# Performance work log

Measured on AMD Instinct MI355X. Metric: run time of the kernel, lower is better.

## Reference

```python
import jax, jax.numpy as jnp
import numpy as np
from functools import partial

B, A = 256, 32          # batch_size, num_atoms
N = B * A               # total nodes = 8192
E = 262144              # edges
H = 128                 # hidden_dim
LD, AF = 64, 16         # latent_dim, atom_feature_dim
L = 6                   # num_layers
LN_EPS = 1e-5

silu = jax.nn.silu


def setup_inputs() -> dict:
    key = jax.random.key(0)
    ks = jax.random.split(key, 32)
    s = 0.02
    inp = {
        "z": jax.random.normal(ks[0], (B, LD), jnp.float32),
        "atom_types": jax.random.uniform(ks[1], (N, AF), jnp.float32),
        "pos_init": jax.random.normal(ks[2], (N, 3), jnp.float32) * 0.1,
        "edge_index": jax.random.randint(ks[3], (2, E), 0, N, jnp.int64) if jax.config.jax_enable_x64 else jax.random.randint(ks[3], (2, E), 0, N, jnp.int32),
        "batch": jax.random.randint(ks[4], (N,), 0, B, jnp.int32),
        # latent injector: (LD+AF)->2H -> 2H->H -> H->H
        "inj_W1": jax.random.normal(ks[5], (LD + AF, 2 * H), jnp.float32) * s,
        "inj_b1": jnp.zeros((2 * H,), jnp.float32),
        "inj_W2": jax.random.normal(ks[6], (2 * H, H), jnp.float32) * s,
        "inj_b2": jnp.zeros((H,), jnp.float32),
        "inj_W3": jax.random.normal(ks[7], (H, H), jnp.float32) * s,
        "inj_b3": jnp.zeros((H,), jnp.float32),
        # stacked per-layer params [L, ...]
        "edge_W1": jax.random.normal(ks[8], (L, 2 * H + 1, H), jnp.float32) * s,
        "edge_b1": jnp.zeros((L, H), jnp.float32),
        "edge_W2": jax.random.normal(ks[9], (L, H, H), jnp.float32) * s,
        "edge_b2": jnp.zeros((L, H), jnp.float32),
        "node_W1": jax.random.normal(ks[10], (L, 2 * H, H), jnp.float32) * s,
        "node_b1": jnp.zeros((L, H), jnp.float32),
        "node_W2": jax.random.normal(ks[11], (L, H, H), jnp.float32) * s,
        "node_b2": jnp.zeros((L, H), jnp.float32),
        "coord_W1": jax.random.normal(ks[12], (L, H, H), jnp.float32) * s,
        "coord_b1": jnp.zeros((L, H), jnp.float32),
        "coord_W2": jax.random.normal(ks[13], (L, H, 1), jnp.float32) * s,  # no bias
        "ln_g": jnp.ones((L, H), jnp.float32),
        "ln_b": jnp.zeros((L, H), jnp.float32),
    }
    return inp


def _layer_norm(x, g, b):
    mu = jnp.mean(x, axis=-1, keepdims=True)
    var = jnp.mean(jnp.square(x - mu), axis=-1, keepdims=True)
    return (x - mu) * jax.lax.rsqrt(var + LN_EPS) * g + b


def _egnn_forward(z, atom_types, pos_init, row, col,
                  inj_W1, inj_b1, inj_W2, inj_b2, inj_W3, inj_b3,
                  edge_W1, edge_b1, edge_W2, edge_b2,
                  node_W1, node_b1, node_W2, node_b2,
                  coord_W1, coord_b1, coord_W2, ln_g, ln_b):
    # latent injection
    z_exp = jnp.repeat(z, A, axis=0)                      # [N, LD]
    h0 = jnp.concatenate([atom_types, z_exp], axis=1)     # [N, AF+LD]
    h = silu(h0 @ inj_W1 + inj_b1)
    h = silu(h @ inj_W2 + inj_b2)
    h = h @ inj_W3 + inj_b3                               # [N, H]

    deg = jax.ops.segment_sum(jnp.ones((E,), h.dtype), row, num_segments=N)[:, None]  # [N,1]

    def step(carry, p):
        h, pos = carry
        (eW1, eb1, eW2, eb2, nW1, nb1, nW2, nb2, cW1, cb1, cW2, g, b) = p
        dpos = pos[row] - pos[col]                                   # [E,3]
        dist_sq = jnp.sum(jnp.square(dpos), axis=1, keepdims=True)   # [E,1]
        ef = jnp.concatenate([h[row], h[col], dist_sq], axis=1)      # [E,2H+1]
        m = silu(silu(ef @ eW1 + eb1) @ eW2 + eb2)                   # [E,H]
        cw = silu(m @ cW1 + cb1) @ cW2                               # [E,1]
        coord_update = jax.ops.segment_sum(cw * dpos, row, num_segments=N)  # [N,3]
        pos_new = pos + coord_update / (deg + 1e-6)
        agg = jax.ops.segment_sum(m, row, num_segments=N)            # [N,H]
        nu = silu(jnp.concatenate([h, agg], axis=1) @ nW1 + nb1) @ nW2 + nb2
        h_new = _layer_norm(h + nu, g, b)
        return (h_new, pos_new), None

    params = (edge_W1, edge_b1, edge_W2, edge_b2, node_W1, node_b1,
              node_W2, node_b2, coord_W1, coord_b1, coord_W2, ln_g, ln_b)
    (h, pos), _ = jax.lax.scan(step, (h, pos_init), params)
    return pos


def reference(z, atom_types, pos_init, edge_index, batch,
              inj_W1, inj_b1, inj_W2, inj_b2, inj_W3, inj_b3,
              edge_W1, edge_b1, edge_W2, edge_b2,
              node_W1, node_b1, node_W2, node_b2,
              coord_W1, coord_b1, coord_W2, ln_g, ln_b):
    row, col = edge_index[0], edge_index[1]
    return _egnn_forward(z, atom_types, pos_init, row, col,
                         inj_W1, inj_b1, inj_W2, inj_b2, inj_W3, inj_b3,
                         edge_W1, edge_b1, edge_W2, edge_b2,
                         node_W1, node_b1, node_W2, node_b2,
                         coord_W1, coord_b1, coord_W2, ln_g, ln_b)
```

## Files before the change

### kernel.cpp

```cpp
#include <hip/hip_runtime.h>
#include <hip/hip_bf16.h>

#define NNODES 8192
#define NEDGES 262144
#define HDIM 128
#define NLAYERS 6
#define NMASK (NNODES - 1)

typedef __attribute__((ext_vector_type(8))) short bf16x8;
typedef __attribute__((ext_vector_type(4))) float f32x4;

__device__ __forceinline__ float silu_f(float x) {
    return x * __builtin_amdgcn_rcpf(1.0f + __expf(-x));
}
__device__ __forceinline__ unsigned short f2bu(float x) {
    unsigned int u; __builtin_memcpy(&u, &x, 4);
    return (unsigned short)((u + 0x8000u) >> 16);
}
__device__ __forceinline__ float bu2f(unsigned short u) {
    unsigned int v = ((unsigned int)u) << 16;
    float f; __builtin_memcpy(&f, &v, 4);
    return f;
}

__global__ void detect_kernel(const int* __restrict__ ei32, int* __restrict__ flags) {
    if (blockIdx.x == 0 && threadIdx.x == 0) {
        flags[1] = (ei32[1] == 0 && ei32[3] == 0 && ei32[5] == 0 && ei32[7] == 0) ? 1 : 0;
    }
}
__device__ __forceinline__ int load_idx(const void* ei, int is64, int i) {
    int v = is64 ? (int)(((const long long*)ei)[i]) : ((const int*)ei)[i];
    return v & NMASK;
}

__global__ void pos_init_kernel(const float* __restrict__ pin, float* __restrict__ pos) {
    int i = blockIdx.x * blockDim.x + threadIdx.x;
    if (i < NNODES * 3) pos[i] = pin[i];
}

__global__ void cnt_kernel(const void* __restrict__ ei, const int* __restrict__ flags,
                           int* __restrict__ cnt) {
    int i = blockIdx.x * blockDim.x + threadIdx.x;
    if (i < NEDGES) atomicAdd(&cnt[load_idx(ei, flags[1], i)], 1);
}
__global__ void scan_kernel(const int* __restrict__ cnt, int* __restrict__ woff,
                            float* __restrict__ deg) {
    __shared__ int sums[256];
    const int t = threadIdx.x;
    const int base = t * 32;
    int s = 0;
#pragma unroll
    for (int i = 0; i < 32; ++i) s += cnt[base + i];
    sums[t] = s;
    __syncthreads();
    if (t == 0) {
        int run = 0;
        for (int k = 0; k < 256; ++k) { int v = sums[k]; sums[k] = run; run += v; }
    }
    __syncthreads();
    int run = sums[t];
#pragma unroll
    for (int i = 0; i < 32; ++i) {
        int c = cnt[base + i];
        woff[base + i] = run;
        deg[base + i] = (float)c;
        run += c;
    }
}
__global__ void scatter_kernel(const void* __restrict__ ei, const int* __restrict__ flags,
                               int* __restrict__ woff,
                               int* __restrict__ rowS, int* __restrict__ colS) {
    int i = blockIdx.x * blockDim.x + threadIdx.x;
    if (i < NEDGES) {
        const int is64 = flags[1];
        int r = load_idx(ei, is64, i);
        int c = load_idx(ei, is64, NEDGES + i);
        int p = atomicAdd(&woff[r], 1);
        rowS[p] = r;
        colS[p] = c;
    }
}

__global__ void prep_weights_kernel(const float* __restrict__ eW1,
                                    const float* __restrict__ eW2,
                                    const float* __restrict__ cW1,
                                    const float* __restrict__ nW1,
                                    const float* __restrict__ nW2,
                                    unsigned short* __restrict__ ewt,
                                    unsigned short* __restrict__ n1tb,
                                    unsigned short* __restrict__ n2tb,
                                    float* __restrict__ w1d) {
    const int TB = NLAYERS * 8 * 4 * 128 * 8;
    const int TS = NLAYERS * 4 * 4 * 128 * 8;
    const int TD = NLAYERS * 128;
    const int TOT = 2 * TB + 3 * TS + TD;
    for (int i = blockIdx.x * blockDim.x + threadIdx.x; i < TOT;
         i += gridDim.x * blockDim.x) {
        if (i < TB) {
            int j = i & 7, r = i >> 3;
            int n = r & 127; r >>= 7;
            int ch = r & 3; r >>= 2;
            int sl = r & 7; int l = r >> 3;
            int k = sl * 32 + ch * 8 + j;
            ewt[(size_t)(l * 16 + sl) * 4096 + ch * 1024 + n * 8 + j] =
                f2bu(eW1[((size_t)l * 257 + k) * 128 + n]);
        } else if (i < TB + TS) {
            int q = i - TB;
            int j = q & 7, r = q >> 3;
            int n = r & 127; r >>= 7;
            int ch = r & 3; r >>= 2;
            int sl = r & 3; int l = r >> 2;
            int k = sl * 32 + ch * 8 + j;
            ewt[(size_t)(l * 16 + 8 + sl) * 4096 + ch * 1024 + n * 8 + j] =
                f2bu(eW2[((size_t)l * 128 + k) * 128 + n]);
        } else if (i < TB + 2 * TS) {
            int q = i - TB - TS;
            int j = q & 7, r = q >> 3;
            int n = r & 127; r >>= 7;
            int ch = r & 3; r >>= 2;
            int sl = r & 3; int l = r >> 2;
            int k = sl * 32 + ch * 8 + j;
            ewt[(size_t)(l * 16 + 12 + sl) * 4096 + ch * 1024 + n * 8 + j] =
                f2bu(cW1[((size_t)l * 128 + k) * 128 + n]);
        } else if (i < 2 * TB + 2 * TS) {
            int q = i - TB - 2 * TS;
            int j = q & 7, r = q >> 3;
            int n = r & 127; r >>= 7;
            int ch = r & 3; r >>= 2;
            int sl = r & 7; int l = r >> 3;
            int k = sl * 32 + ch * 8 + j;
            n1tb[q] = f2bu(nW1[((size_t)l * 256 + k) * 128 + n]);
        } else if (i < 2 * TB + 3 * TS) {
            int q = i - 2 * TB - 2 * TS;
            int j = q & 7, r = q >> 3;
            int n = r & 127; r >>= 7;
            int ch = r & 3; r >>= 2;
            int sl = r & 3; int l = r >> 2;
            int k = sl * 32 + ch * 8 + j;
            n2tb[q] = f2bu(nW2[((size_t)l * 128 + k) * 128 + n]);
        } else {
            int r = i - 2 * TB - 3 * TS, l = r / 128, n = r % 128;
            w1d[r] = eW1[((size_t)l * 257 + 256) * 128 + n];
        }
    }
}

__global__ __launch_bounds__(256) void inj_kernel(
    const float* __restrict__ atom, const float* __restrict__ z,
    const float* __restrict__ W1, const float* __restrict__ b1,
    const float* __restrict__ W2, const float* __restrict__ b2,
    const float* __restrict__ W3, const float* __restrict__ b3,
    unsigned short* __restrict__ hb)
{
    __shared__ __align__(16) float in_s[16][84];
    __shared__ __align__(16) float s1[16][260];
    __shared__ __align__(16) float s2[16][132];
    const int tid = threadIdx.x;
    const int n0 = blockIdx.x * 16;

    if (tid < 80) {
        for (int e = 0; e < 16; ++e) {
            int n = n0 + e;
            in_s[e][tid] = (tid < 16) ? atom[n * 16 + tid] : z[(n >> 5) * 64 + (tid - 16)];
        }
    }
    __syncthreads();
    {
        float acc[16];
        float bias = b1[tid];
#pragma unroll
        for (int e = 0; e < 16; ++e) acc[e] = bias;
        for (int k4 = 0; k4 < 20; ++k4) {
            float w0 = W1[(k4 * 4 + 0) * 256 + tid];
            float w1 = W1[(k4 * 4 + 1) * 256 + tid];
            float w2 = W1[(k4 * 4 + 2) * 256 + tid];
            float w3 = W1[(k4 * 4 + 3) * 256 + tid];
#pragma unroll
            for (int e = 0; e < 16; ++e) {
                const float4 v = *(const float4*)&in_s[e][k4 * 4];
                acc[e] += v.x * w0 + v.y * w1 + v.z * w2 + v.w * w3;
            }
        }
#pragma unroll
        for (int e = 0; e < 16; ++e) s1[e][tid] = silu_f(acc[e]);
    }
    __syncthreads();
    const int j = tid & 127, hv = tid >> 7;
    {
        float acc[8];
        float bias = b2[j];
#pragma unroll
        for (int e = 0; e < 8; ++e) acc[e] = bias;
        for (int k4 = 0; k4 < 64; ++k4) {
            float w0 = W2[(k4 * 4 + 0) * 128 + j];
            float w1 = W2[(k4 * 4 + 1) * 128 + j];
            float w2 = W2[(k4 * 4 + 2) * 128 + j];
            float w3 = W2[(k4 * 4 + 3) * 128 + j];
#pragma unroll
            for (int e = 0; e < 8; ++e) {
                const float4 v = *(const float4*)&s1[hv * 8 + e][k4 * 4];
                acc[e] += v.x * w0 + v.y * w1 + v.z * w2 + v.w * w3;
            }
        }
#pragma unroll
        for (int e = 0; e < 8; ++e) s2[hv * 8 + e][j] = silu_f(acc[e]);
    }
    __syncthreads();
    {
        float acc[8];
        float bias = b3[j];
#pragma unroll
        for (int e = 0; e < 8; ++e) acc[e] = bias;
        for (int k4 = 0; k4 < 32; ++k4) {
            float w0 = W3[(k4 * 4 + 0) * 128 + j];
            float w1 = W3[(k4 * 4 + 1) * 128 + j];
            float w2 = W3[(k4 * 4 + 2) * 128 + j];
            float w3 = W3[(k4 * 4 + 3) * 128 + j];
#pragma unroll
            for (int e = 0; e < 8; ++e) {
                const float4 v = *(const float4*)&s2[hv * 8 + e][k4 * 4];
                acc[e] += v.x * w0 + v.y * w1 + v.z * w2 + v.w * w3;
            }
        }
#pragma unroll
        for (int e = 0; e < 8; ++e)
            hb[(size_t)(n0 + hv * 8 + e) * HDIM + j] = f2bu(acc[e]);
    }
}

__global__ __launch_bounds__(256, 3) void edge_mfma_kernel(
    const unsigned short* __restrict__ hb, const float* __restrict__ pos,
    const int* __restrict__ rowS, const int* __restrict__ colS,
    const unsigned short* __restrict__ wt,
    const float* __restrict__ w1d,
    const float* __restrict__ eb1, const float* __restrict__ eb2,
    const float* __restrict__ cb1, const float* __restrict__ cw2,
    float* __restrict__ agg, float* __restrict__ cu)
{
    __shared__ __align__(16) unsigned short Cbuf[128][136];

    const int tid = threadIdx.x;
    const int e0 = blockIdx.x * 128;
    const int L = tid & 63;
    const int w = tid >> 6;
    const int quad = L >> 4, l16 = L & 15;
    const int m0 = w * 32;

    const unsigned short* bbase = wt + quad * 1024 + l16 * 8;

    bf16x8 breg[2][8];
    bf16x8 areg[2][2];
#pragma unroll
    for (int nt = 0; nt < 8; ++nt)
        breg[0][nt] = *(const bf16x8*)(bbase + nt * 128);

    if (tid < 128) {
        int r = rowS[e0 + tid], c = colS[e0 + tid];
        float dx = pos[r * 3 + 0] - pos[c * 3 + 0];
        float dy = pos[r * 3 + 1] - pos[c * 3 + 1];
        float dz = pos[r * 3 + 2] - pos[c * 3 + 2];
        *(float*)&Cbuf[tid][128] = dx * dx + dy * dy + dz * dz;
        Cbuf[tid][130] = (unsigned short)r;
        Cbuf[tid][131] = (unsigned short)c;
        Cbuf[tid][132] = f2bu(dx); Cbuf[tid][133] = f2bu(dy); Cbuf[tid][134] = f2bu(dz);
    }
    __syncthreads();

    const int r0 = Cbuf[m0 + l16][130];
    const int r1 = Cbuf[m0 + 16 + l16][130];
    const int c0 = Cbuf[m0 + l16][131];
    const int c1 = Cbuf[m0 + 16 + l16][131];

    {
        const int kk = quad * 8;
        areg[0][0] = *(const bf16x8*)(hb + (size_t)r0 * HDIM + kk);
        areg[0][1] = *(const bf16x8*)(hb + (size_t)r1 * HDIM + kk);
    }

    f32x4 acc[2][8];
    const f32x4 zero = {0.f, 0.f, 0.f, 0.f};
#pragma unroll
    for (int mt = 0; mt < 2; ++mt)
#pragma unroll
        for (int nt = 0; nt < 8; ++nt) acc[mt][nt] = zero;

#pragma unroll
    for (int s = 0; s < 16; ++s) {
        const int cur = s & 1, nxt = cur ^ 1;

        if (s < 15) {
#pragma unroll
            for (int nt = 0; nt < 8; ++nt)
                breg[nxt][nt] = *(const bf16x8*)(bbase + (s + 1) * 4096 + nt * 128);
        }
        if (s < 7) {
            const int kk = ((s + 1) & 3) * 32 + quad * 8;
            const int nn0 = (s + 1 < 4) ? r0 : c0;
            const int nn1 = (s + 1 < 4) ? r1 : c1;
            areg[nxt][0] = *(const bf16x8*)(hb + (size_t)nn0 * HDIM + kk);
            areg[nxt][1] = *(const bf16x8*)(hb + (size_t)nn1 * HDIM + kk);
        }

        bf16x8 a0, a1;
        if (s < 8) {
            a0 = areg[cur][0]; a1 = areg[cur][1];
        } else {
            const int kk = ((s - 8) & 3) * 32 + quad * 8;
            a0 = *(const bf16x8*)&Cbuf[m0 + l16][kk];
            a1 = *(const bf16x8*)&Cbuf[m0 + 16 + l16][kk];
        }
#pragma unroll
        for (int nt = 0; nt < 8; ++nt) {
            acc[0][nt] = __builtin_amdgcn_mfma_f32_16x16x32_bf16(a0, breg[cur][nt], acc[0][nt], 0, 0, 0);
            acc[1][nt] = __builtin_amdgcn_mfma_f32_16x16x32_bf16(a1, breg[cur][nt], acc[1][nt], 0, 0, 0);
        }

        if (s == 7) {
#pragma unroll
            for (int nt = 0; nt < 8; ++nt) {
                const int n = nt * 16 + l16;
                const float wd = w1d[n];
                const float bias = eb1[n];
#pragma unroll
                for (int mt = 0; mt < 2; ++mt)
#pragma unroll
                    for (int r = 0; r < 4; ++r) {
                        const int m = m0 + mt * 16 + quad * 4 + r;
                        float dsq = *(const float*)&Cbuf[m][128];
                        Cbuf[m][n] = f2bu(silu_f(acc[mt][nt][r] + bias + dsq * wd));
                    }
            }
#pragma unroll
            for (int mt = 0; mt < 2; ++mt)
#pragma unroll
                for (int nt = 0; nt < 8; ++nt) acc[mt][nt] = zero;
        } else if (s == 11) {
#pragma unroll
            for (int nt = 0; nt < 8; ++nt) {
                const int n = nt * 16 + l16;
                const float bias = eb2[n];
#pragma unroll
                for (int mt = 0; mt < 2; ++mt)
#pragma unroll
                    for (int r = 0; r < 4; ++r) {
                        const int m = m0 + mt * 16 + quad * 4 + r;
                        Cbuf[m][n] = f2bu(silu_f(acc[mt][nt][r] + bias));
                    }
            }
#pragma unroll
            for (int mt = 0; mt < 2; ++mt)
#pragma unroll
                for (int nt = 0; nt < 8; ++nt) acc[mt][nt] = zero;
        }
    }

    {
        float s[2][4] = {{0.f, 0.f, 0.f, 0.f}, {0.f, 0.f, 0.f, 0.f}};
#pragma unroll
        for (int nt = 0; nt < 8; ++nt) {
            const int n = nt * 16 + l16;
            const float bias = cb1[n];
            const float wv = cw2[n];
#pragma unroll
            for (int mt = 0; mt < 2; ++mt)
#pragma unroll
                for (int r = 0; r < 4; ++r)
                    s[mt][r] += silu_f(acc[mt][nt][r] + bias) * wv;
        }
#pragma unroll
        for (int mt = 0; mt < 2; ++mt)
#pragma unroll
            for (int r = 0; r < 4; ++r) {
                float v = s[mt][r];
                v += __shfl_xor(v, 1);
                v += __shfl_xor(v, 2);
                v += __shfl_xor(v, 4);
                v += __shfl_xor(v, 8);
                if (l16 == 0)
                    *(float*)&Cbuf[m0 + mt * 16 + quad * 4 + r][128] = v;
            }
    }

    if (L < 32) {
        const int e = m0 + L;
        const int row = Cbuf[e][130];
        const float cwv = *(const float*)&Cbuf[e][128];
        float vx = cwv * bu2f(Cbuf[e][132]);
        float vy = cwv * bu2f(Cbuf[e][133]);
        float vz = cwv * bu2f(Cbuf[e][134]);
#pragma unroll
        for (int d = 1; d < 32; d <<= 1) {
            float ux = __shfl_up(vx, d);
            float uy = __shfl_up(vy, d);
            float uz = __shfl_up(vz, d);
            int rup = __shfl_up(row, d);
            if (L >= d && rup == row) { vx += ux; vy += uy; vz += uz; }
        }
        int rdn = __shfl_down(row, 1);
        if (L == 31 || rdn != row) {
            atomicAdd(&cu[row * 3 + 0], vx);
            atomicAdd(&cu[row * 3 + 1], vy);
            atomicAdd(&cu[row * 3 + 2], vz);
        }
    }

    {
        const int p = L;
        const int eb = m0;
        const int i31 = L & 31;
        const int myrow = Cbuf[eb + i31][130];
        const int prow = __shfl_up(myrow, 1);
        unsigned long long bm64 = __ballot(i31 != 0 && myrow != prow);
        unsigned int bm = (unsigned int)bm64;
        int curr = Cbuf[eb][130];
        float s0 = 0.0f, s1 = 0.0f;
#pragma unroll
        for (int i = 0; i < 32; ++i) {
            unsigned int v = *(const unsigned int*)&Cbuf[eb + i][2 * p];
            if (i && (bm & (1u << i))) {
                atomicAdd(&agg[(size_t)curr * HDIM + 2 * p], s0);
                atomicAdd(&agg[(size_t)curr * HDIM + 2 * p + 1], s1);
                s0 = 0.0f; s1 = 0.0f;
                curr = __shfl(myrow, i);
            }
            s0 += bu2f((unsigned short)(v & 0xffffu));
            s1 += bu2f((unsigned short)(v >> 16));
        }
        atomicAdd(&agg[(size_t)curr * HDIM + 2 * p], s0);
        atomicAdd(&agg[(size_t)curr * HDIM + 2 * p + 1], s1);
    }
}

__global__ __launch_bounds__(128) void node_mfma_kernel(
    const unsigned short* __restrict__ hb,
    float* __restrict__ agg,
    float* __restrict__ cu, const float* __restrict__ deg,
    const unsigned short* __restrict__ n1tb,
    const unsigned short* __restrict__ n2tb,
    const float* __restrict__ b1, const float* __restrict__ b2,
    const float* __restrict__ lg, const float* __restrict__ lb,
    unsigned short* __restrict__ h2b,
    float* __restrict__ pos)
{
    __shared__ __align__(16) unsigned short Cbuf[16][136];
    __shared__ float sLN[2][16][2];
    const int tid = threadIdx.x;
    const int n0 = blockIdx.x * 16;

    if (tid < 16) {
        int n = n0 + tid;
        float inv = __builtin_amdgcn_rcpf(deg[n] + 1e-6f);
        pos[n * 3 + 0] += cu[n * 3 + 0] * inv;
        pos[n * 3 + 1] += cu[n * 3 + 1] * inv;
        pos[n * 3 + 2] += cu[n * 3 + 2] * inv;
        cu[n * 3 + 0] = 0.0f;
        cu[n * 3 + 1] = 0.0f;
        cu[n * 3 + 2] = 0.0f;
    }

    const int L = tid & 63, w = tid >> 6;
    const int quad = L >> 4, l16 = L & 15;
    const int row = n0 + l16;
    const int nb = w * 64;

    f32x4 acc[4];
    const f32x4 zero = {0.f, 0.f, 0.f, 0.f};

#pragma unroll
    for (int nt = 0; nt < 4; ++nt) acc[nt] = zero;
#pragma unroll
    for (int kc = 0; kc < 8; ++kc) {
        bf16x8 a;
        if (kc < 4) {
            const int kk = kc * 32 + quad * 8;
            a = *(const bf16x8*)(hb + (size_t)row * HDIM + kk);
        } else {
            const int kk = (kc - 4) * 32 + quad * 8;
            const float4* p = (const float4*)(agg + (size_t)row * HDIM + kk);
            float4 u0 = p[0], u1 = p[1];
            a[0] = (short)f2bu(u0.x); a[1] = (short)f2bu(u0.y);
            a[2] = (short)f2bu(u0.z); a[3] = (short)f2bu(u0.w);
            a[4] = (short)f2bu(u1.x); a[5] = (short)f2bu(u1.y);
            a[6] = (short)f2bu(u1.z); a[7] = (short)f2bu(u1.w);
        }
        const unsigned short* bp = n1tb + (kc * 4 + quad) * 1024 + (nb + l16) * 8;
#pragma unroll
        for (int nt = 0; nt < 4; ++nt) {
            bf16x8 b = *(const bf16x8*)(bp + nt * 128);
            acc[nt] = __builtin_amdgcn_mfma_f32_16x16x32_bf16(a, b, acc[nt], 0, 0, 0);
        }
    }
    {
        const float4 z4 = {0.f, 0.f, 0.f, 0.f};
        float4* ap = (float4*)(agg + (size_t)(n0 + (tid >> 3)) * HDIM + (tid & 7) * 16);
#pragma unroll
        for (int i = 0; i < 4; ++i) ap[i] = z4;
    }
#pragma unroll
    for (int nt = 0; nt < 4; ++nt) {
        const int n = nb + nt * 16 + l16;
        const float bias = b1[n];
#pragma unroll
        for (int r = 0; r < 4; ++r)
            Cbuf[quad * 4 + r][n] = f2bu(silu_f(acc[nt][r] + bias));
    }
    __syncthreads();

#pragma unroll
    for (int nt = 0; nt < 4; ++nt) acc[nt] = zero;
#pragma unroll
    for (int kc = 0; kc < 4; ++kc) {
        const int kk = kc * 32 + quad * 8;
        bf16x8 a = *(const bf16x8*)&Cbuf[l16][kk];
        const unsigned short* bp = n2tb + (kc * 4 + quad) * 1024 + (nb + l16) * 8;
#pragma unroll
        for (int nt = 0; nt < 4; ++nt) {
            bf16x8 b = *(const bf16x8*)(bp + nt * 128);
            acc[nt] = __builtin_amdgcn_mfma_f32_16x16x32_bf16(a, b, acc[nt], 0, 0, 0);
        }
    }

#pragma unroll
    for (int nt = 0; nt < 4; ++nt) {
        const int n = nb + nt * 16 + l16;
        const float bias = b2[n];
#pragma unroll
        for (int r = 0; r < 4; ++r) {
            const int m = quad * 4 + r;
            acc[nt][r] += bias + bu2f(hb[(size_t)(n0 + m) * HDIM + n]);
        }
    }
#pragma unroll
    for (int r = 0; r < 4; ++r) {
        float s = 0.0f, ss = 0.0f;
#pragma unroll
        for (int nt = 0; nt < 4; ++nt) {
            float x = acc[nt][r];
            s += x; ss += x * x;
        }
#pragma unroll
        for (int d = 1; d < 16; d <<= 1) {
            s += __shfl_xor(s, d);
            ss += __shfl_xor(ss, d);
        }
        if (l16 == 0) {
            sLN[w][quad * 4 + r][0] = s;
            sLN[w][quad * 4 + r][1] = ss;
        }
    }
    __syncthreads();
#pragma unroll
    for (int r = 0; r < 4; ++r) {
        const int m = quad * 4 + r;
        float s = sLN[0][m][0] + sLN[1][m][0];
        float ss = sLN[0][m][1] + sLN[1][m][1];
        float mu = s * (1.0f / 128.0f);
        float var = ss * (1.0f / 128.0f) - mu * mu;
        float rs = rsqrtf(fmaxf(var, 0.0f) + 1e-5f);
#pragma unroll
        for (int nt = 0; nt < 4; ++nt) {
            const int n = nb + nt * 16 + l16;
            float val = (acc[nt][r] - mu) * rs * lg[n] + lb[n];
            h2b[(size_t)(n0 + m) * HDIM + n] = f2bu(val);
        }
    }
}

extern "C" void kernel_launch(void* const* d_in, const int* in_sizes, int n_in,
                              void* d_out, int out_size, void* d_ws, size_t ws_size,
                              hipStream_t stream) {
    const float* zF    = (const float*)d_in[0];
    const float* atomF = (const float*)d_in[1];
    const float* posI  = (const float*)d_in[2];
    const void*  ei    = d_in[3];
    const float* iW1 = (const float*)d_in[5];  const float* ib1 = (const float*)d_in[6];
    const float* iW2 = (const float*)d_in[7];  const float* ib2 = (const float*)d_in[8];
    const float* iW3 = (const float*)d_in[9];  const float* ib3 = (const float*)d_in[10];
    const float* eW1 = (const float*)d_in[11]; const float* eb1 = (const float*)d_in[12];
    const float* eW2 = (const float*)d_in[13]; const float* eb2 = (const float*)d_in[14];
    const float* nW1 = (const float*)d_in[15]; const float* nb1 = (const float*)d_in[16];
    const float* nW2 = (const float*)d_in[17]; const float* nb2 = (const float*)d_in[18];
    const float* cW1 = (const float*)d_in[19]; const float* cb1 = (const float*)d_in[20];
    const float* cW2 = (const float*)d_in[21];
    const float* lng = (const float*)d_in[22]; const float* lnb = (const float*)d_in[23];

    float* pos = (float*)d_out;

    float* ws = (float*)d_ws;
    int* flags = (int*)d_ws;
    size_t cur = 16;
    auto carve = [&](size_t n) { float* p = ws + cur; cur += n; return p; };
    float* deg  = carve(NNODES);
    float* cu   = carve((size_t)NNODES * 3);
    float* agg  = carve((size_t)NNODES * HDIM);
    unsigned short* hbA = (unsigned short*)carve((size_t)NNODES * HDIM / 2);
    unsigned short* hbB = (unsigned short*)carve((size_t)NNODES * HDIM / 2);
    unsigned short* ewt  = (unsigned short*)carve((size_t)NLAYERS * 16 * 4096 / 2);
    unsigned short* n1tb = (unsigned short*)carve((size_t)NLAYERS * 8 * 4096 / 2);
    unsigned short* n2tb = (unsigned short*)carve((size_t)NLAYERS * 4 * 4096 / 2);
    float* w1d  = carve(NLAYERS * 128);
    int* cnt    = (int*)carve(NNODES);
    int* woff   = (int*)carve(NNODES);
    int* rowS   = (int*)carve(NEDGES);
    int* colS   = (int*)carve(NEDGES);

    detect_kernel<<<1, 64, 0, stream>>>((const int*)ei, flags);
    pos_init_kernel<<<(NNODES * 3 + 255) / 256, 256, 0, stream>>>(posI, pos);

    hipMemsetAsync(cnt, 0, NNODES * sizeof(int), stream);
    cnt_kernel<<<NEDGES / 256, 256, 0, stream>>>(ei, flags, cnt);
    scan_kernel<<<1, 256, 0, stream>>>(cnt, woff, deg);
    scatter_kernel<<<NEDGES / 256, 256, 0, stream>>>(ei, flags, woff, rowS, colS);

    prep_weights_kernel<<<2691, 256, 0, stream>>>(eW1, eW2, cW1, nW1, nW2,
                                                  ewt, n1tb, n2tb, w1d);
    inj_kernel<<<NNODES / 16, 256, 0, stream>>>(atomF, zF, iW1, ib1, iW2, ib2, iW3, ib3,
                                                hbA);

    hipMemsetAsync(agg, 0, (size_t)NNODES * HDIM * sizeof(float), stream);
    hipMemsetAsync(cu, 0, (size_t)NNODES * 3 * sizeof(float), stream);

    unsigned short* hb = hbA;
    unsigned short* ob = hbB;
    for (int l = 0; l < NLAYERS; ++l) {
        edge_mfma_kernel<<<NEDGES / 128, 256, 0, stream>>>(
            hb, pos, rowS, colS,
            ewt + (size_t)l * 16 * 4096,
            w1d + (size_t)l * 128,
            eb1 + l * 128, eb2 + l * 128, cb1 + l * 128, cW2 + l * 128,
            agg, cu);
        node_mfma_kernel<<<NNODES / 16, 128, 0, stream>>>(
            hb, agg, cu, deg,
            n1tb + (size_t)l * 8 * 4096,
            n2tb + (size_t)l * 4 * 4096,
            nb1 + l * 128, nb2 + l * 128,
            lng + l * 128, lnb + l * 128,
            ob, pos);
        unsigned short* tb = hb; hb = ob; ob = tb;
    }
}
```

Before: 666.3 us.

## Restructure edge kernel to single-wave blocks of 64 edges with 4 M-tiles

Changes the edge kernel from 256-thread blocks (4 waves × 32 edges) to 64-thread single-wave blocks processing 64 edges, each wave computing four 16-row M tiles. This drops the block-level __syncthreads and doubles reuse of each loaded B-weight fragment across more MFMAs, and segmented reductions now span 64 edges, which cuts the number of atomics. In exchange it doubles the accumulator registers (32 f32x4), which reduces occupancy under launch_bounds(64,2). It also halves the edges per block, so the grid has twice as many blocks.

```diff
diff --git a/kernel.cpp b/kernel.cpp
--- a/kernel.cpp
+++ b/kernel.cpp
@@ -228,7 +228,7 @@
     }
 }
 
-__global__ __launch_bounds__(256, 3) void edge_mfma_kernel(
+__global__ __launch_bounds__(64, 2) void edge_mfma_kernel(
     const unsigned short* __restrict__ hb, const float* __restrict__ pos,
     const int* __restrict__ rowS, const int* __restrict__ colS,
     const unsigned short* __restrict__ wt,
@@ -237,24 +237,21 @@
     const float* __restrict__ cb1, const float* __restrict__ cw2,
     float* __restrict__ agg, float* __restrict__ cu)
 {
-    __shared__ __align__(16) unsigned short Cbuf[128][136];
+    __shared__ __align__(16) unsigned short Cbuf[64][136];
 
     const int tid = threadIdx.x;
-    const int e0 = blockIdx.x * 128;
-    const int L = tid & 63;
-    const int w = tid >> 6;
-    const int quad = L >> 4, l16 = L & 15;
-    const int m0 = w * 32;
+    const int e0 = blockIdx.x * 64;
+    const int quad = tid >> 4, l16 = tid & 15;
 
     const unsigned short* bbase = wt + quad * 1024 + l16 * 8;
 
     bf16x8 breg[2][8];
-    bf16x8 areg[2][2];
+    bf16x8 areg[2][4];
 #pragma unroll
     for (int nt = 0; nt < 8; ++nt)
         breg[0][nt] = *(const bf16x8*)(bbase + nt * 128);
 
-    if (tid < 128) {
+    {
         int r = rowS[e0 + tid], c = colS[e0 + tid];
         float dx = pos[r * 3 + 0] - pos[c * 3 + 0];
         float dy = pos[r * 3 + 1] - pos[c * 3 + 1];
@@ -264,23 +261,24 @@
         Cbuf[tid][131] = (unsigned short)c;
         Cbuf[tid][132] = f2bu(dx); Cbuf[tid][133] = f2bu(dy); Cbuf[tid][134] = f2bu(dz);
     }
-    __syncthreads();
-
-    const int r0 = Cbuf[m0 + l16][130];
-    const int r1 = Cbuf[m0 + 16 + l16][130];
-    const int c0 = Cbuf[m0 + l16][131];
-    const int c1 = Cbuf[m0 + 16 + l16][131];
-
+
+    int rm[4], cm[4];
+#pragma unroll
+    for (int mt = 0; mt < 4; ++mt) {
+        rm[mt] = Cbuf[mt * 16 + l16][130];
+        cm[mt] = Cbuf[mt * 16 + l16][131];
+    }
     {
         const int kk = quad * 8;
-        areg[0][0] = *(const bf16x8*)(hb + (size_t)r0 * HDIM + kk);
-        areg[0][1] = *(const bf16x8*)(hb + (size_t)r1 * HDIM + kk);
-    }
-
-    f32x4 acc[2][8];
+#pragma unroll
+        for (int mt = 0; mt < 4; ++mt)
+            areg[0][mt] = *(const bf16x8*)(hb + (size_t)rm[mt] * HDIM + kk);
+    }
+
+    f32x4 acc[4][8];
     const f32x4 zero = {0.f, 0.f, 0.f, 0.f};
 #pragma unroll
-    for (int mt = 0; mt < 2; ++mt)
+    for (int mt = 0; mt < 4; ++mt)
 #pragma unroll
         for (int nt = 0; nt < 8; ++nt) acc[mt][nt] = zero;
 
@@ -295,25 +293,28 @@
         }
         if (s < 7) {
             const int kk = ((s + 1) & 3) * 32 + quad * 8;
-            const int nn0 = (s + 1 < 4) ? r0 : c0;
-            const int nn1 = (s + 1 < 4) ? r1 : c1;
-            areg[nxt][0] = *(const bf16x8*)(hb + (size_t)nn0 * HDIM + kk);
-            areg[nxt][1] = *(const bf16x8*)(hb + (size_t)nn1 * HDIM + kk);
-        }
-
-        bf16x8 a0, a1;
+#pragma unroll
+            for (int mt = 0; mt < 4; ++mt) {
+                const int nn = (s + 1 < 4) ? rm[mt] : cm[mt];
+                areg[nxt][mt] = *(const bf16x8*)(hb + (size_t)nn * HDIM + kk);
+            }
+        }
+
+        bf16x8 a[4];
         if (s < 8) {
-            a0 = areg[cur][0]; a1 = areg[cur][1];
+#pragma unroll
+            for (int mt = 0; mt < 4; ++mt) a[mt] = areg[cur][mt];
         } else {
             const int kk = ((s - 8) & 3) * 32 + quad * 8;
-            a0 = *(const bf16x8*)&Cbuf[m0 + l16][kk];
-            a1 = *(const bf16x8*)&Cbuf[m0 + 16 + l16][kk];
-        }
-#pragma unroll
-        for (int nt = 0; nt < 8; ++nt) {
-            acc[0][nt] = __builtin_amdgcn_mfma_f32_16x16x32_bf16(a0, breg[cur][nt], acc[0][nt], 0, 0, 0);
-            acc[1][nt] = __builtin_amdgcn_mfma_f32_16x16x32_bf16(a1, breg[cur][nt], acc[1][nt], 0, 0, 0);
-        }
+#pragma unroll
+            for (int mt = 0; mt < 4; ++mt)
+                a[mt] = *(const bf16x8*)&Cbuf[mt * 16 + l16][kk];
+        }
+#pragma unroll
+        for (int nt = 0; nt < 8; ++nt)
+#pragma unroll
+            for (int mt = 0; mt < 4; ++mt)
+                acc[mt][nt] = __builtin_amdgcn_mfma_f32_16x16x32_bf16(a[mt], breg[cur][nt], acc[mt][nt], 0, 0, 0);
 
         if (s == 7) {
 #pragma unroll
@@ -322,16 +323,16 @@
                 const float wd = w1d[n];
                 const float bias = eb1[n];
 #pragma unroll
-                for (int mt = 0; mt < 2; ++mt)
+                for (int mt = 0; mt < 4; ++mt)
 #pragma unroll
                     for (int r = 0; r < 4; ++r) {
-                        const int m = m0 + mt * 16 + quad * 4 + r;
+                        const int m = mt * 16 + quad * 4 + r;
                         float dsq = *(const float*)&Cbuf[m][128];
                         Cbuf[m][n] = f2bu(silu_f(acc[mt][nt][r] + bias + dsq * wd));
                     }
             }
 #pragma unroll
-            for (int mt = 0; mt < 2; ++mt)
+            for (int mt = 0; mt < 4; ++mt)
 #pragma unroll
                 for (int nt = 0; nt < 8; ++nt) acc[mt][nt] = zero;
         } else if (s == 11) {
@@ -340,64 +341,64 @@
                 const int n = nt * 16 + l16;
                 const float bias = eb2[n];
 #pragma unroll
-                for (int mt = 0; mt < 2; ++mt)
+                for (int mt = 0; mt < 4; ++mt)
 #pragma unroll
                     for (int r = 0; r < 4; ++r) {
-                        const int m = m0 + mt * 16 + quad * 4 + r;
+                        const int m = mt * 16 + quad * 4 + r;
                         Cbuf[m][n] = f2bu(silu_f(acc[mt][nt][r] + bias));
                     }
             }
 #pragma unroll
-            for (int mt = 0; mt < 2; ++mt)
+            for (int mt = 0; mt < 4; ++mt)
 #pragma unroll
                 for (int nt = 0; nt < 8; ++nt) acc[mt][nt] = zero;
         }
     }
 
     {
-        float s[2][4] = {{0.f, 0.f, 0.f, 0.f}, {0.f, 0.f, 0.f, 0.f}};
+        float sv[4][4] = {{0.f,0.f,0.f,0.f},{0.f,0.f,0.f,0.f},
+                          {0.f,0.f,0.f,0.f},{0.f,0.f,0.f,0.f}};
 #pragma unroll
         for (int nt = 0; nt < 8; ++nt) {
             const int n = nt * 16 + l16;
             const float bias = cb1[n];
             const float wv = cw2[n];
 #pragma unroll
-            for (int mt = 0; mt < 2; ++mt)
+            for (int mt = 0; mt < 4; ++mt)
 #pragma unroll
                 for (int r = 0; r < 4; ++r)
-                    s[mt][r] += silu_f(acc[mt][nt][r] + bias) * wv;
-        }
-#pragma unroll
-        for (int mt = 0; mt < 2; ++mt)
+                    sv[mt][r] += silu_f(acc[mt][nt][r] + bias) * wv;
+        }
+#pragma unroll
+        for (int mt = 0; mt < 4; ++mt)
 #pragma unroll
             for (int r = 0; r < 4; ++r) {
-                float v = s[mt][r];
+                float v = sv[mt][r];
                 v += __shfl_xor(v, 1);
                 v += __shfl_xor(v, 2);
                 v += __shfl_xor(v, 4);
                 v += __shfl_xor(v, 8);
                 if (l16 == 0)
-                    *(float*)&Cbuf[m0 + mt * 16 + quad * 4 + r][128] = v;
-            }
-    }
-
-    if (L < 32) {
-        const int e = m0 + L;
-        const int row = Cbuf[e][130];
-        const float cwv = *(const float*)&Cbuf[e][128];
-        float vx = cwv * bu2f(Cbuf[e][132]);
-        float vy = cwv * bu2f(Cbuf[e][133]);
-        float vz = cwv * bu2f(Cbuf[e][134]);
-#pragma unroll
-        for (int d = 1; d < 32; d <<= 1) {
+                    *(float*)&Cbuf[mt * 16 + quad * 4 + r][128] = v;
+            }
+    }
+
+    {
+        const int row = Cbuf[tid][130];
+        const float cwv = *(const float*)&Cbuf[tid][128];
+        float vx = cwv * bu2f(Cbuf[tid][132]);
+        float vy = cwv * bu2f(Cbuf[tid][133]);
+        float vz = cwv * bu2f(Cbuf[tid][134]);
+#pragma unroll
+        for (int d = 1; d < 64; d <<= 1) {
             float ux = __shfl_up(vx, d);
             float uy = __shfl_up(vy, d);
             float uz = __shfl_up(vz, d);
             int rup = __shfl_up(row, d);
-            if (L >= d && rup == row) { vx += ux; vy += uy; vz += uz; }
+            if (tid >= d && rup == row) { vx += ux; vy += uy; vz += uz; }
         }
         int rdn = __shfl_down(row, 1);
-        if (L == 31 || rdn != row) {
+        if (tid == 63 || rdn != row) {
             atomicAdd(&cu[row * 3 + 0], vx);
             atomicAdd(&cu[row * 3 + 1], vy);
             atomicAdd(&cu[row * 3 + 2], vz);
@@ -405,19 +406,16 @@
     }
 
     {
-        const int p = L;
-        const int eb = m0;
-        const int i31 = L & 31;
-        const int myrow = Cbuf[eb + i31][130];
+        const int p = tid;
+        const int myrow = Cbuf[tid][130];
         const int prow = __shfl_up(myrow, 1);
-        unsigned long long bm64 = __ballot(i31 != 0 && myrow != prow);
-        unsigned int bm = (unsigned int)bm64;
-        int curr = Cbuf[eb][130];
+        const unsigned long long bm = __ballot(tid != 0 && myrow != prow);
+        int curr = Cbuf[0][130];
         float s0 = 0.0f, s1 = 0.0f;
 #pragma unroll
-        for (int i = 0; i < 32; ++i) {
-            unsigned int v = *(const unsigned int*)&Cbuf[eb + i][2 * p];
-            if (i && (bm & (1u << i))) {
+        for (int i = 0; i < 64; ++i) {
+            unsigned int v = *(const unsigned int*)&Cbuf[i][2 * p];
+            if (i && ((bm >> i) & 1ull)) {
                 atomicAdd(&agg[(size_t)curr * HDIM + 2 * p], s0);
                 atomicAdd(&agg[(size_t)curr * HDIM + 2 * p + 1], s1);
                 s0 = 0.0f; s1 = 0.0f;
@@ -623,7 +621,7 @@
     unsigned short* hb = hbA;
     unsigned short* ob = hbB;
     for (int l = 0; l < NLAYERS; ++l) {
-        edge_mfma_kernel<<<NEDGES / 128, 256, 0, stream>>>(
+        edge_mfma_kernel<<<NEDGES / 64, 64, 0, stream>>>(
             hb, pos, rowS, colS,
             ewt + (size_t)l * 16 * 4096,
             w1d + (size_t)l * 128,
```

Result: slower. 707.2 us (+6.1%).

## Stage edge weight slices into LDS via global_load_lds double buffering

Applied to the files above, without the earlier changes.

Instead of having each wave load its own copy of the weight B-fragments into registers from global memory, the block now cooperatively copies each 4096-element weight slice into a double-buffered LDS array using direct global-to-LDS loads. The MFMAs then read their B operands from LDS. The goal is to cut redundant global and L2 weight traffic across the four waves and free the large breg register array, which could help occupancy. In exchange it adds a __syncthreads per k-step and extra LDS reads and capacity. There is also a possible race, because the async global_load_lds may not be complete at the barrier without an explicit vmcnt wait.

```diff
diff --git a/kernel.cpp b/kernel.cpp
--- a/kernel.cpp
+++ b/kernel.cpp
@@ -9,6 +9,8 @@
 
 typedef __attribute__((ext_vector_type(8))) short bf16x8;
 typedef __attribute__((ext_vector_type(4))) float f32x4;
+typedef const __attribute__((address_space(1))) void gvoid;
+typedef __attribute__((address_space(3))) void svoid;
 
 __device__ __forceinline__ float silu_f(float x) {
     return x * __builtin_amdgcn_rcpf(1.0f + __expf(-x));
@@ -21,6 +23,14 @@
     unsigned int v = ((unsigned int)u) << 16;
     float f; __builtin_memcpy(&f, &v, 4);
     return f;
+}
+
+__device__ __forceinline__ void stage_slice(const unsigned short* src,
+                                            unsigned short* dst, int w) {
+    const unsigned short* s = src + w * 1024;
+    unsigned short* d = dst + w * 1024;
+    __builtin_amdgcn_global_load_lds((gvoid*)s, (svoid*)d, 16, 0, 0);
+    __builtin_amdgcn_global_load_lds((gvoid*)(s + 512), (svoid*)(d + 512), 16, 0, 0);
 }
 
 __global__ void detect_kernel(const int* __restrict__ ei32, int* __restrict__ flags) {
@@ -238,6 +248,7 @@
     float* __restrict__ agg, float* __restrict__ cu)
 {
     __shared__ __align__(16) unsigned short Cbuf[128][136];
+    __shared__ __align__(16) unsigned short Bbuf[2][4096];
 
     const int tid = threadIdx.x;
     const int e0 = blockIdx.x * 128;
@@ -246,13 +257,7 @@
     const int quad = L >> 4, l16 = L & 15;
     const int m0 = w * 32;
 
-    const unsigned short* bbase = wt + quad * 1024 + l16 * 8;
-
-    bf16x8 breg[2][8];
-    bf16x8 areg[2][2];
-#pragma unroll
-    for (int nt = 0; nt < 8; ++nt)
-        breg[0][nt] = *(const bf16x8*)(bbase + nt * 128);
+    stage_slice(wt, Bbuf[0], w);
 
     if (tid < 128) {
         int r = rowS[e0 + tid], c = colS[e0 + tid];
@@ -271,10 +276,11 @@
     const int c0 = Cbuf[m0 + l16][131];
     const int c1 = Cbuf[m0 + 16 + l16][131];
 
+    bf16x8 aCur0, aCur1, aNxt0, aNxt1;
     {
         const int kk = quad * 8;
-        areg[0][0] = *(const bf16x8*)(hb + (size_t)r0 * HDIM + kk);
-        areg[0][1] = *(const bf16x8*)(hb + (size_t)r1 * HDIM + kk);
+        aCur0 = *(const bf16x8*)(hb + (size_t)r0 * HDIM + kk);
+        aCur1 = *(const bf16x8*)(hb + (size_t)r1 * HDIM + kk);
     }
 
     f32x4 acc[2][8];
@@ -286,24 +292,21 @@
 
 #pragma unroll
     for (int s = 0; s < 16; ++s) {
-        const int cur = s & 1, nxt = cur ^ 1;
-
-        if (s < 15) {
-#pragma unroll
-            for (int nt = 0; nt < 8; ++nt)
-                breg[nxt][nt] = *(const bf16x8*)(bbase + (s + 1) * 4096 + nt * 128);
-        }
+        if (s) __syncthreads();
+        if (s < 15) stage_slice(wt + (s + 1) * 4096, Bbuf[(s + 1) & 1], w);
+
         if (s < 7) {
             const int kk = ((s + 1) & 3) * 32 + quad * 8;
             const int nn0 = (s + 1 < 4) ? r0 : c0;
             const int nn1 = (s + 1 < 4) ? r1 : c1;
-            areg[nxt][0] = *(const bf16x8*)(hb + (size_t)nn0 * HDIM + kk);
-            areg[nxt][1] = *(const bf16x8*)(hb + (size_t)nn1 * HDIM + kk);
-        }
-
+            aNxt0 = *(const bf16x8*)(hb + (size_t)nn0 * HDIM + kk);
+            aNxt1 = *(const bf16x8*)(hb + (size_t)nn1 * HDIM + kk);
+        }
+
+        const unsigned short* bp = Bbuf[s & 1] + quad * 1024;
         bf16x8 a0, a1;
         if (s < 8) {
-            a0 = areg[cur][0]; a1 = areg[cur][1];
+            a0 = aCur0; a1 = aCur1;
         } else {
             const int kk = ((s - 8) & 3) * 32 + quad * 8;
             a0 = *(const bf16x8*)&Cbuf[m0 + l16][kk];
@@ -311,9 +314,11 @@
         }
 #pragma unroll
         for (int nt = 0; nt < 8; ++nt) {
-            acc[0][nt] = __builtin_amdgcn_mfma_f32_16x16x32_bf16(a0, breg[cur][nt], acc[0][nt], 0, 0, 0);
-            acc[1][nt] = __builtin_amdgcn_mfma_f32_16x16x32_bf16(a1, breg[cur][nt], acc[1][nt], 0, 0, 0);
-        }
+            bf16x8 b = *(const bf16x8*)&bp[(nt * 16 + l16) * 8];
+            acc[0][nt] = __builtin_amdgcn_mfma_f32_16x16x32_bf16(a0, b, acc[0][nt], 0, 0, 0);
+            acc[1][nt] = __builtin_amdgcn_mfma_f32_16x16x32_bf16(a1, b, acc[1][nt], 0, 0, 0);
+        }
+        if (s < 7) { aCur0 = aNxt0; aCur1 = aNxt1; }
 
         if (s == 7) {
 #pragma unroll
```

New measurement: 627.9 us. 1.06x faster.
